# Kernel optimization log

Measured on AMD Instinct MI355X. Metric: run time of the kernel, lower is better.

The kernel has to match this reference:

```python
import jax, jax.numpy as jnp
import numpy as np

N_NODES = 50000
N_EDGES = 800000
IN_CH = 64
OUT_CH = 64
PRIOR_VAR = 1.0


def setup_inputs() -> dict:
    key = jax.random.key(0)
    ks = jax.random.split(key, 10)
    mean = jax.random.normal(ks[0], (N_NODES, IN_CH), dtype=jnp.float32)
    std = jax.random.uniform(ks[1], (N_NODES, IN_CH), dtype=jnp.float32)
    edge_index = jax.random.randint(ks[2], (2, N_EDGES), 0, N_NODES, dtype=jnp.int32)
    edge_weight = jax.random.uniform(ks[3], (N_EDGES,), dtype=jnp.float32)
    # Bayesian GCN parameters (xavier-ish mu, log_sigma init -3.0) for mean- and std-branches
    scale = float(np.sqrt(6.0 / (IN_CH + OUT_CH)))
    mu_mean = jax.random.uniform(ks[4], (IN_CH, OUT_CH), minval=-scale, maxval=scale, dtype=jnp.float32)
    log_sigma_mean = jnp.full((IN_CH, OUT_CH), -3.0, dtype=jnp.float32)
    mu_std = jax.random.uniform(ks[5], (IN_CH, OUT_CH), minval=-scale, maxval=scale, dtype=jnp.float32)
    log_sigma_std = jnp.full((IN_CH, OUT_CH), -3.0, dtype=jnp.float32)
    # reparameterization noise (drawn once so reference is deterministic)
    eps_mean = jax.random.normal(ks[6], (IN_CH, OUT_CH), dtype=jnp.float32)
    eps_std = jax.random.normal(ks[7], (IN_CH, OUT_CH), dtype=jnp.float32)
    return {
        "mean": mean, "std": std, "edge_index": edge_index, "edge_weight": edge_weight,
        "mu_mean": mu_mean, "log_sigma_mean": log_sigma_mean, "eps_mean": eps_mean,
        "mu_std": mu_std, "log_sigma_std": log_sigma_std, "eps_std": eps_std,
    }


def _gcn_propagate(x, weight, edge_index, edge_weight):
    # support = x @ W; then gather src rows, scale by edge_weight, scatter-add to dst
    support = jnp.matmul(x, weight)                      # [N, out]
    src, dst = edge_index[0], edge_index[1]
    msg = edge_weight[:, None] * support[src]            # [E, out]
    return jax.ops.segment_sum(msg, dst, num_segments=N_NODES)


def _kl(mu, log_sigma):
    pv = PRIOR_VAR
    kl = 0.5 * (jnp.exp(2.0 * log_sigma) / pv + mu ** 2 / pv
                - 2.0 * log_sigma - jnp.log(jnp.asarray(pv, mu.dtype)) - 1.0)
    return kl.sum()


def reference(mean, std, edge_index, edge_weight,
              mu_mean, log_sigma_mean, eps_mean,
              mu_std, log_sigma_std, eps_std):
    # mean branch
    w_mean = mu_mean + eps_mean * jnp.exp(log_sigma_mean)
    new_mean = _gcn_propagate(mean, w_mean, edge_index, edge_weight)
    kl_mean = _kl(mu_mean, log_sigma_mean)
    # std branch operates on variance with squared edge weights
    var = std ** 2
    w_std = mu_std + eps_std * jnp.exp(log_sigma_std)
    new_log_var = _gcn_propagate(var, w_std, edge_index, edge_weight ** 2)
    kl_std = _kl(mu_std, log_sigma_std)
    new_std = jnp.sqrt(jnp.exp(new_log_var) + 1e-6)
    total_kl = kl_mean + kl_std
    return (new_mean, new_std, total_kl)
```

## Files before the change

kernel.cpp:

```cpp
#include <hip/hip_runtime.h>

#define N_NODES 50000
#define N_EDGES 800000
#define CH 64
#define OUT_OFF_STD (N_NODES * CH)
#define OUT_OFF_KL  (2 * N_NODES * CH)
#define CAP 64
#define CAP_USE 62

#define NGRP 8
#define NPG 6250
#define FILL_CHUNK 4096
#define FILL_CHUNKS 196
#define FILL_BLOCKS (NGRP * FILL_CHUNKS)
#define GEMM_BLOCKS 782
#define GATHER_BLOCKS 2048
#define GWAVES_PG 1024
#define ZERO_GRID 208

typedef __attribute__((ext_vector_type(8))) short short8;
typedef __attribute__((ext_vector_type(4))) float f32x4;

__device__ __forceinline__ int rl_i(unsigned v, int lane) {
    return __builtin_amdgcn_readlane((int)v, lane);
}
__device__ __forceinline__ unsigned f2bf(float f) {
    unsigned u = __float_as_uint(f);
    return (u + 0x7fffu + ((u >> 16) & 1u)) >> 16;
}
__device__ __forceinline__ int* cnt_ptr(uint2* bins, int node) {
    return (int*)(bins + (size_t)node * CAP + 63);
}

__global__ __launch_bounds__(256) void wkl_kernel(
    const float* __restrict__ mu_m, const float* __restrict__ ls_m,
    const float* __restrict__ eps_m,
    const float* __restrict__ mu_s, const float* __restrict__ ls_s,
    const float* __restrict__ eps_s,
    unsigned short* __restrict__ fragBm, unsigned short* __restrict__ fragBv,
    float* __restrict__ kl_out, uint2* __restrict__ bins)
{
    if (blockIdx.x != 0) {
        if (blockIdx.x < 8) return;
        const int g = blockIdx.x & (NGRP - 1);
        const int loc = ((int)(blockIdx.x >> 3) - 1) * 256 + (int)threadIdx.x;
        if (loc < NPG) *cnt_ptr(bins, g * NPG + loc) = 0;
        return;
    }
    __shared__ unsigned short Wm[CH * CH];
    __shared__ unsigned short Wv[CH * CH];
    float kl = 0.0f;
    for (int i = threadIdx.x; i < CH * CH; i += 256) {
        float mu = mu_m[i], ls = ls_m[i];
        Wm[i] = (unsigned short)f2bf(mu + eps_m[i] * expf(ls));
        kl += 0.5f * (expf(2.0f * ls) + mu * mu - 2.0f * ls - 1.0f);
        mu = mu_s[i]; ls = ls_s[i];
        Wv[i] = (unsigned short)f2bf(mu + eps_s[i] * expf(ls));
        kl += 0.5f * (expf(2.0f * ls) + mu * mu - 2.0f * ls - 1.0f);
    }
    __syncthreads();
    for (int f = threadIdx.x; f < CH * CH; f += 256) {
        int j = f & 7, l = (f >> 3) & 63, ch = f >> 9;
        int k = (ch & 1) * 32 + ((l >> 4) & 3) * 8 + j;
        int n = (ch >> 1) * 16 + (l & 15);
        fragBm[f] = Wm[k * CH + n];
        fragBv[f] = Wv[k * CH + n];
    }
    for (int off = 32; off > 0; off >>= 1)
        kl += __shfl_down(kl, off, 64);
    __shared__ float red[4];
    if ((threadIdx.x & 63) == 0) red[threadIdx.x >> 6] = kl;
    __syncthreads();
    if (threadIdx.x == 0)
        kl_out[0] = red[0] + red[1] + red[2] + red[3];
}

__global__ __launch_bounds__(256) void gemfill_kernel(
    const float* __restrict__ mean, const float* __restrict__ stdv,
    const unsigned short* __restrict__ fragBm,
    const unsigned short* __restrict__ fragBv,
    const int* __restrict__ ei, const float* __restrict__ ew,
    uint2* __restrict__ bins, unsigned* __restrict__ sup)
{
    const int tid = threadIdx.x;

    if (blockIdx.x < FILL_BLOCKS) {
        const int g = blockIdx.x & (NGRP - 1);
        const int chunk = blockIdx.x >> 3;
        const int base = chunk * FILL_CHUNK + tid * 16;
        const int lo = g * NPG;

        int d[16], s[16]; float w[16];
        if (base + 16 <= N_EDGES) {
#pragma unroll
            for (int h = 0; h < 4; ++h) {
                int4 dv = *(const int4*)(ei + N_EDGES + base + h * 4);
                d[h * 4 + 0] = dv.x; d[h * 4 + 1] = dv.y;
                d[h * 4 + 2] = dv.z; d[h * 4 + 3] = dv.w;
            }
#pragma unroll
            for (int h = 0; h < 4; ++h) {
                int4 sv = *(const int4*)(ei + base + h * 4);
                s[h * 4 + 0] = sv.x; s[h * 4 + 1] = sv.y;
                s[h * 4 + 2] = sv.z; s[h * 4 + 3] = sv.w;
            }
#pragma unroll
            for (int h = 0; h < 4; ++h) {
                float4 wv = *(const float4*)(ew + base + h * 4);
                w[h * 4 + 0] = wv.x; w[h * 4 + 1] = wv.y;
                w[h * 4 + 2] = wv.z; w[h * 4 + 3] = wv.w;
            }
        } else {
#pragma unroll
            for (int t = 0; t < 16; ++t) {
                bool v = (base + t) < N_EDGES;
                d[t] = v ? ei[N_EDGES + base + t] : -1;
                s[t] = v ? ei[base + t] : 0;
                w[t] = v ? ew[base + t] : 0.0f;
            }
        }

        int slot[16];
#pragma unroll
        for (int t = 0; t < 16; ++t) {
            bool act = (unsigned)(d[t] - lo) < (unsigned)NPG;
            slot[t] = act ? atomicAdd(cnt_ptr(bins, d[t]), 1) : CAP;
        }
#pragma unroll
        for (int t = 0; t < 16; ++t) {
            if (slot[t] < CAP_USE)
                bins[(size_t)d[t] * CAP + slot[t]] =
                    make_uint2((unsigned)s[t], __float_as_uint(w[t]));
        }
        return;
    }

    const int lane = tid & 63, wave = tid >> 6;
    const int row0 = (blockIdx.x - FILL_BLOCKS) * 64 + wave * 16;
    if (row0 >= N_NODES) return;

    const int m = lane & 15;
    const int q = (lane >> 4) & 3;
    const float* mrow = mean + (size_t)(row0 + m) * CH + q * 8;
    const float* srow = stdv + (size_t)(row0 + m) * CH + q * 8;

    short8 aM[2], aV[2];
#pragma unroll
    for (int h = 0; h < 2; ++h) {
        float4 x0 = *(const float4*)(mrow + h * 32);
        float4 x1 = *(const float4*)(mrow + h * 32 + 4);
        float4 s0 = *(const float4*)(srow + h * 32);
        float4 s1 = *(const float4*)(srow + h * 32 + 4);
        aM[h][0] = (short)f2bf(x0.x); aM[h][1] = (short)f2bf(x0.y);
        aM[h][2] = (short)f2bf(x0.z); aM[h][3] = (short)f2bf(x0.w);
        aM[h][4] = (short)f2bf(x1.x); aM[h][5] = (short)f2bf(x1.y);
        aM[h][6] = (short)f2bf(x1.z); aM[h][7] = (short)f2bf(x1.w);
        aV[h][0] = (short)f2bf(s0.x * s0.x); aV[h][1] = (short)f2bf(s0.y * s0.y);
        aV[h][2] = (short)f2bf(s0.z * s0.z); aV[h][3] = (short)f2bf(s0.w * s0.w);
        aV[h][4] = (short)f2bf(s1.x * s1.x); aV[h][5] = (short)f2bf(s1.y * s1.y);
        aV[h][6] = (short)f2bf(s1.z * s1.z); aV[h][7] = (short)f2bf(s1.w * s1.w);
    }

    f32x4 accM[4], accV[4];
#pragma unroll
    for (int c = 0; c < 4; ++c) {
        accM[c] = (f32x4)0.0f;
        accV[c] = (f32x4)0.0f;
    }
#pragma unroll
    for (int c = 0; c < 4; ++c) {
#pragma unroll
        for (int h = 0; h < 2; ++h) {
            short8 bm = *(const short8*)(fragBm + ((c * 2 + h) * 64 + lane) * 8);
            short8 bv = *(const short8*)(fragBv + ((c * 2 + h) * 64 + lane) * 8);
            accM[c] = __builtin_amdgcn_mfma_f32_16x16x32_bf16(aM[h], bm, accM[c], 0, 0, 0);
            accV[c] = __builtin_amdgcn_mfma_f32_16x16x32_bf16(aV[h], bv, accV[c], 0, 0, 0);
        }
    }

    const int rg = lane >> 4;
#pragma unroll
    for (int c = 0; c < 4; ++c) {
#pragma unroll
        for (int r = 0; r < 4; ++r) {
            int node = row0 + rg * 4 + r;
            sup[(size_t)node * CH + c * 16 + m] =
                f2bf(accM[c][r]) | (f2bf(accV[c][r]) << 16);
        }
    }
}

__global__ __launch_bounds__(256) void gather_kernel(
    const uint2* __restrict__ bins,
    const unsigned* __restrict__ sup, float* __restrict__ out)
{
    const int g = blockIdx.x & (NGRP - 1);
    const int wid = ((int)(blockIdx.x >> 3)) * 4 + (int)(threadIdx.x >> 6);
    const int col = threadIdx.x & 63;
    const int nbase = g * NPG;

    int loc = wid;
    if (loc >= NPG) return;

    uint2 pnext = bins[(size_t)(nbase + loc) * CAP + col];

    for (; loc < NPG; loc += GWAVES_PG) {
        uint2 p = pnext;
        {
            int loc2 = loc + GWAVES_PG;
            if (loc2 < NPG)
                pnext = bins[(size_t)(nbase + loc2) * CAP + col];
        }
        int cnt = rl_i(p.x, 63);
        if (cnt > CAP_USE) cnt = CAP_USE;

        float accM = 0.0f, accV = 0.0f;
        if (cnt > 0) {
            unsigned q[24];
#pragma unroll
            for (int t = 0; t < 24; ++t) {
                int e = (t < cnt) ? t : (cnt - 1);
                q[t] = sup[(size_t)(unsigned)rl_i(p.x, e) * CH + col];
            }
#pragma unroll
            for (int t = 0; t < 24; ++t) {
                int e = (t < cnt) ? t : (cnt - 1);
                float wt = (t < cnt)
                    ? __uint_as_float((unsigned)rl_i(p.y, e)) : 0.0f;
                accM += wt * __uint_as_float(q[t] << 16);
                accV += (wt * wt) * __uint_as_float(q[t] & 0xFFFF0000u);
            }
            for (int i = 24; i < cnt; i += 8) {
                unsigned qq[8]; float ww[8];
#pragma unroll
                for (int t = 0; t < 8; ++t) {
                    int e = (i + t < cnt) ? (i + t) : (cnt - 1);
                    qq[t] = sup[(size_t)(unsigned)rl_i(p.x, e) * CH + col];
                    ww[t] = (i + t < cnt)
                        ? __uint_as_float((unsigned)rl_i(p.y, e)) : 0.0f;
                }
#pragma unroll
                for (int t = 0; t < 8; ++t) {
                    accM += ww[t] * __uint_as_float(qq[t] << 16);
                    accV += (ww[t] * ww[t]) * __uint_as_float(qq[t] & 0xFFFF0000u);
                }
            }
        }
        const int n = nbase + loc;
        __builtin_nontemporal_store(accM, &out[(size_t)n * CH + col]);
        __builtin_nontemporal_store(sqrtf(expf(accV) + 1e-6f),
                                    &out[OUT_OFF_STD + (size_t)n * CH + col]);
    }
}

extern "C" void kernel_launch(void* const* d_in, const int* in_sizes, int n_in,
                              void* d_out, int out_size, void* d_ws, size_t ws_size,
                              hipStream_t stream)
{
    const float* mean  = (const float*)d_in[0];
    const float* stdv  = (const float*)d_in[1];
    const int*   ei    = (const int*)d_in[2];
    const float* ew    = (const float*)d_in[3];
    const float* mu_m  = (const float*)d_in[4];
    const float* ls_m  = (const float*)d_in[5];
    const float* eps_m = (const float*)d_in[6];
    const float* ls_s  = (const float*)d_in[8];
    const float* mu_s  = (const float*)d_in[7];
    const float* eps_s = (const float*)d_in[9];

    float* out = (float*)d_out;
    unsigned*       sup    = (unsigned*)d_ws;
    uint2*          bins   = (uint2*)(sup + (size_t)N_NODES * CH);
    unsigned short* fragBm = (unsigned short*)(bins + (size_t)N_NODES * CAP);
    unsigned short* fragBv = fragBm + CH * CH;

    wkl_kernel<<<ZERO_GRID, 256, 0, stream>>>(
        mu_m, ls_m, eps_m, mu_s, ls_s, eps_s,
        fragBm, fragBv, out + OUT_OFF_KL, bins);
    gemfill_kernel<<<FILL_BLOCKS + GEMM_BLOCKS, 256, 0, stream>>>(
        mean, stdv, fragBm, fragBv, ei, ew, bins, sup);
    gather_kernel<<<GATHER_BLOCKS, 256, 0, stream>>>(bins, sup, out);
}
```

Measured before the change: 174.4 us.

## Fuse three kernels into one persistent cooperative kernel with grid syncs

```diff
diff --git a/kernel.cpp b/kernel.cpp
--- a/kernel.cpp
+++ b/kernel.cpp
@@ -1,4 +1,7 @@
 #include <hip/hip_runtime.h>
+#include <hip/hip_cooperative_groups.h>
+
+namespace cg = cooperative_groups;
 
 #define N_NODES 50000
 #define N_EDGES 800000
@@ -10,13 +13,10 @@
 
 #define NGRP 8
 #define NPG 6250
-#define FILL_CHUNK 4096
-#define FILL_CHUNKS 196
-#define FILL_BLOCKS (NGRP * FILL_CHUNKS)
-#define GEMM_BLOCKS 782
-#define GATHER_BLOCKS 2048
-#define GWAVES_PG 1024
-#define ZERO_GRID 208
+#define FILL_CHUNK 2048
+#define FILL_CHUNKS 391
+#define GEMM_TILES 782
+#define MAX_BLOCKS 1536
 
 typedef __attribute__((ext_vector_type(8))) short short8;
 typedef __attribute__((ext_vector_type(4))) float f32x4;
@@ -32,224 +32,221 @@
     return (int*)(bins + (size_t)node * CAP + 63);
 }
 
-__global__ __launch_bounds__(256) void wkl_kernel(
+__global__ __launch_bounds__(256, 6) void fused_kernel(
+    const float* __restrict__ mean, const float* __restrict__ stdv,
+    const int* __restrict__ ei, const float* __restrict__ ew,
     const float* __restrict__ mu_m, const float* __restrict__ ls_m,
     const float* __restrict__ eps_m,
     const float* __restrict__ mu_s, const float* __restrict__ ls_s,
     const float* __restrict__ eps_s,
     unsigned short* __restrict__ fragBm, unsigned short* __restrict__ fragBv,
-    float* __restrict__ kl_out, uint2* __restrict__ bins)
+    uint2* __restrict__ bins, unsigned* __restrict__ sup,
+    int* __restrict__ qcnt, float* __restrict__ out)
 {
-    if (blockIdx.x != 0) {
-        if (blockIdx.x < 8) return;
-        const int g = blockIdx.x & (NGRP - 1);
-        const int loc = ((int)(blockIdx.x >> 3) - 1) * 256 + (int)threadIdx.x;
-        if (loc < NPG) *cnt_ptr(bins, g * NPG + loc) = 0;
-        return;
+    cg::grid_group grid = cg::this_grid();
+    const int tid = threadIdx.x;
+    const int bid = (int)blockIdx.x;
+    const int nblk = (int)gridDim.x;
+
+    __shared__ float red[4];
+    __shared__ int sh_chunk;
+
+    if (bid == 0) {
+        float kl = 0.0f;
+        for (int i = tid; i < CH * CH; i += 256) {
+            float mu = mu_m[i], ls = ls_m[i];
+            kl += 0.5f * (expf(2.0f * ls) + mu * mu - 2.0f * ls - 1.0f);
+            mu = mu_s[i]; ls = ls_s[i];
+            kl += 0.5f * (expf(2.0f * ls) + mu * mu - 2.0f * ls - 1.0f);
+        }
+        for (int off = 32; off > 0; off >>= 1)
+            kl += __shfl_down(kl, off, 64);
+        if ((tid & 63) == 0) red[tid >> 6] = kl;
+        __syncthreads();
+        if (tid == 0)
+            out[OUT_OFF_KL] = red[0] + red[1] + red[2] + red[3];
+    } else {
+        const int p = (bid - 1) * 256 + tid;
+        const int pstride = (nblk - 1) * 256;
+        for (int f = p; f < CH * CH; f += pstride) {
+            int j = f & 7, l = (f >> 3) & 63, ch = f >> 9;
+            int k = (ch & 1) * 32 + ((l >> 4) & 3) * 8 + j;
+            int n = (ch >> 1) * 16 + (l & 15);
+            int i = k * CH + n;
+            fragBm[f] = (unsigned short)f2bf(mu_m[i] + eps_m[i] * expf(ls_m[i]));
+            fragBv[f] = (unsigned short)f2bf(mu_s[i] + eps_s[i] * expf(ls_s[i]));
+        }
+        for (int i = p; i < N_NODES; i += pstride)
+            *cnt_ptr(bins, i) = 0;
+        if (p < NGRP * 16) qcnt[p] = 0;
     }
-    __shared__ unsigned short Wm[CH * CH];
-    __shared__ unsigned short Wv[CH * CH];
-    float kl = 0.0f;
-    for (int i = threadIdx.x; i < CH * CH; i += 256) {
-        float mu = mu_m[i], ls = ls_m[i];
-        Wm[i] = (unsigned short)f2bf(mu + eps_m[i] * expf(ls));
-        kl += 0.5f * (expf(2.0f * ls) + mu * mu - 2.0f * ls - 1.0f);
-        mu = mu_s[i]; ls = ls_s[i];
-        Wv[i] = (unsigned short)f2bf(mu + eps_s[i] * expf(ls));
-        kl += 0.5f * (expf(2.0f * ls) + mu * mu - 2.0f * ls - 1.0f);
+    grid.sync();
+
+    const int gb = nblk >> 3;
+    const int fb = nblk - gb;
+    if (bid < fb) {
+        const int g = bid & (NGRP - 1);
+        const int lo = g * NPG;
+        for (;;) {
+            __syncthreads();
+            if (tid == 0) sh_chunk = atomicAdd(&qcnt[g * 16], 1);
+            __syncthreads();
+            const int c = sh_chunk;
+            if (c >= FILL_CHUNKS) break;
+            const int base = c * FILL_CHUNK + tid * 8;
+
+            int d[8], s[8]; float w[8];
+            if (base + 8 <= N_EDGES) {
+                int4 d0 = *(const int4*)(ei + N_EDGES + base);
+                int4 d1 = *(const int4*)(ei + N_EDGES + base + 4);
+                d[0] = d0.x; d[1] = d0.y; d[2] = d0.z; d[3] = d0.w;
+                d[4] = d1.x; d[5] = d1.y; d[6] = d1.z; d[7] = d1.w;
+                int4 s0 = *(const int4*)(ei + base);
+                int4 s1 = *(const int4*)(ei + base + 4);
+                s[0] = s0.x; s[1] = s0.y; s[2] = s0.z; s[3] = s0.w;
+                s[4] = s1.x; s[5] = s1.y; s[6] = s1.z; s[7] = s1.w;
+                float4 w0 = *(const float4*)(ew + base);
+                float4 w1 = *(const float4*)(ew + base + 4);
+                w[0] = w0.x; w[1] = w0.y; w[2] = w0.z; w[3] = w0.w;
+                w[4] = w1.x; w[5] = w1.y; w[6] = w1.z; w[7] = w1.w;
+            } else {
+#pragma unroll
+                for (int t = 0; t < 8; ++t) {
+                    bool v = (base + t) < N_EDGES;
+                    d[t] = v ? ei[N_EDGES + base + t] : -1;
+                    s[t] = v ? ei[base + t] : 0;
+                    w[t] = v ? ew[base + t] : 0.0f;
+                }
+            }
+            int slot[8];
+#pragma unroll
+            for (int t = 0; t < 8; ++t) {
+                bool act = (unsigned)(d[t] - lo) < (unsigned)NPG;
+                slot[t] = act ? atomicAdd(cnt_ptr(bins, d[t]), 1) : CAP;
+            }
+#pragma unroll
+            for (int t = 0; t < 8; ++t) {
+                if (slot[t] < CAP_USE)
+                    bins[(size_t)d[t] * CAP + slot[t]] =
+                        make_uint2((unsigned)s[t], __float_as_uint(w[t]));
+            }
+        }
+    } else {
+        const int lane = tid & 63, wave = tid >> 6;
+        const int m = lane & 15;
+        const int q = (lane >> 4) & 3;
+        const int rg = lane >> 4;
+
+        for (int t = bid - fb; t < GEMM_TILES; t += gb) {
+            const int row0 = t * 64 + wave * 16;
+            if (row0 >= N_NODES) continue;
+            const float* mrow = mean + (size_t)(row0 + m) * CH + q * 8;
+            const float* srow = stdv + (size_t)(row0 + m) * CH + q * 8;
+
+            short8 aM[2], aV[2];
+#pragma unroll
+            for (int h = 0; h < 2; ++h) {
+                float4 x0 = *(const float4*)(mrow + h * 32);
+                float4 x1 = *(const float4*)(mrow + h * 32 + 4);
+                float4 s0 = *(const float4*)(srow + h * 32);
+                float4 s1 = *(const float4*)(srow + h * 32 + 4);
+                aM[h][0] = (short)f2bf(x0.x); aM[h][1] = (short)f2bf(x0.y);
+                aM[h][2] = (short)f2bf(x0.z); aM[h][3] = (short)f2bf(x0.w);
+                aM[h][4] = (short)f2bf(x1.x); aM[h][5] = (short)f2bf(x1.y);
+                aM[h][6] = (short)f2bf(x1.z); aM[h][7] = (short)f2bf(x1.w);
+                aV[h][0] = (short)f2bf(s0.x * s0.x); aV[h][1] = (short)f2bf(s0.y * s0.y);
+                aV[h][2] = (short)f2bf(s0.z * s0.z); aV[h][3] = (short)f2bf(s0.w * s0.w);
+                aV[h][4] = (short)f2bf(s1.x * s1.x); aV[h][5] = (short)f2bf(s1.y * s1.y);
+                aV[h][6] = (short)f2bf(s1.z * s1.z); aV[h][7] = (short)f2bf(s1.w * s1.w);
+            }
+
+            f32x4 accM[4], accV[4];
+#pragma unroll
+            for (int c = 0; c < 4; ++c) {
+                accM[c] = (f32x4)0.0f;
+                accV[c] = (f32x4)0.0f;
+            }
+#pragma unroll
+            for (int c = 0; c < 4; ++c) {
+#pragma unroll
+                for (int h = 0; h < 2; ++h) {
+                    short8 bm = *(const short8*)(fragBm + ((c * 2 + h) * 64 + lane) * 8);
+                    short8 bv = *(const short8*)(fragBv + ((c * 2 + h) * 64 + lane) * 8);
+                    accM[c] = __builtin_amdgcn_mfma_f32_16x16x32_bf16(aM[h], bm, accM[c], 0, 0, 0);
+                    accV[c] = __builtin_amdgcn_mfma_f32_16x16x32_bf16(aV[h], bv, accV[c], 0, 0, 0);
+                }
+            }
+#pragma unroll
+            for (int c = 0; c < 4; ++c) {
+#pragma unroll
+                for (int r = 0; r < 4; ++r) {
+                    int node = row0 + rg * 4 + r;
+                    sup[(size_t)node * CH + c * 16 + m] =
+                        f2bf(accM[c][r]) | (f2bf(accV[c][r]) << 16);
+                }
+            }
+        }
     }
-    __syncthreads();
-    for (int f = threadIdx.x; f < CH * CH; f += 256) {
-        int j = f & 7, l = (f >> 3) & 63, ch = f >> 9;
-        int k = (ch & 1) * 32 + ((l >> 4) & 3) * 8 + j;
-        int n = (ch >> 1) * 16 + (l & 15);
-        fragBm[f] = Wm[k * CH + n];
-        fragBv[f] = Wv[k * CH + n];
-    }
-    for (int off = 32; off > 0; off >>= 1)
-        kl += __shfl_down(kl, off, 64);
-    __shared__ float red[4];
-    if ((threadIdx.x & 63) == 0) red[threadIdx.x >> 6] = kl;
-    __syncthreads();
-    if (threadIdx.x == 0)
-        kl_out[0] = red[0] + red[1] + red[2] + red[3];
-}
-
-__global__ __launch_bounds__(256) void gemfill_kernel(
-    const float* __restrict__ mean, const float* __restrict__ stdv,
-    const unsigned short* __restrict__ fragBm,
-    const unsigned short* __restrict__ fragBv,
-    const int* __restrict__ ei, const float* __restrict__ ew,
-    uint2* __restrict__ bins, unsigned* __restrict__ sup)
-{
-    const int tid = threadIdx.x;
-
-    if (blockIdx.x < FILL_BLOCKS) {
-        const int g = blockIdx.x & (NGRP - 1);
-        const int chunk = blockIdx.x >> 3;
-        const int base = chunk * FILL_CHUNK + tid * 16;
-        const int lo = g * NPG;
-
-        int d[16], s[16]; float w[16];
-        if (base + 16 <= N_EDGES) {
-#pragma unroll
-            for (int h = 0; h < 4; ++h) {
-                int4 dv = *(const int4*)(ei + N_EDGES + base + h * 4);
-                d[h * 4 + 0] = dv.x; d[h * 4 + 1] = dv.y;
-                d[h * 4 + 2] = dv.z; d[h * 4 + 3] = dv.w;
-            }
-#pragma unroll
-            for (int h = 0; h < 4; ++h) {
-                int4 sv = *(const int4*)(ei + base + h * 4);
-                s[h * 4 + 0] = sv.x; s[h * 4 + 1] = sv.y;
-                s[h * 4 + 2] = sv.z; s[h * 4 + 3] = sv.w;
-            }
-#pragma unroll
-            for (int h = 0; h < 4; ++h) {
-                float4 wv = *(const float4*)(ew + base + h * 4);
-                w[h * 4 + 0] = wv.x; w[h * 4 + 1] = wv.y;
-                w[h * 4 + 2] = wv.z; w[h * 4 + 3] = wv.w;
-            }
-        } else {
-#pragma unroll
-            for (int t = 0; t < 16; ++t) {
-                bool v = (base + t) < N_EDGES;
-                d[t] = v ? ei[N_EDGES + base + t] : -1;
-                s[t] = v ? ei[base + t] : 0;
-                w[t] = v ? ew[base + t] : 0.0f;
-            }
-        }
-
-        int slot[16];
-#pragma unroll
-        for (int t = 0; t < 16; ++t) {
-            bool act = (unsigned)(d[t] - lo) < (unsigned)NPG;
-            slot[t] = act ? atomicAdd(cnt_ptr(bins, d[t]), 1) : CAP;
-        }
-#pragma unroll
-        for (int t = 0; t < 16; ++t) {
-            if (slot[t] < CAP_USE)
-                bins[(size_t)d[t] * CAP + slot[t]] =
-                    make_uint2((unsigned)s[t], __float_as_uint(w[t]));
-        }
-        return;
-    }
-
-    const int lane = tid & 63, wave = tid >> 6;
-    const int row0 = (blockIdx.x - FILL_BLOCKS) * 64 + wave * 16;
-    if (row0 >= N_NODES) return;
-
-    const int m = lane & 15;
-    const int q = (lane >> 4) & 3;
-    const float* mrow = mean + (size_t)(row0 + m) * CH + q * 8;
-    const float* srow = stdv + (size_t)(row0 + m) * CH + q * 8;
-
-    short8 aM[2], aV[2];
-#pragma unroll
-    for (int h = 0; h < 2; ++h) {
-        float4 x0 = *(const float4*)(mrow + h * 32);
-        float4 x1 = *(const float4*)(mrow + h * 32 + 4);
-        float4 s0 = *(const float4*)(srow + h * 32);
-        float4 s1 = *(const float4*)(srow + h * 32 + 4);
-        aM[h][0] = (short)f2bf(x0.x); aM[h][1] = (short)f2bf(x0.y);
-        aM[h][2] = (short)f2bf(x0.z); aM[h][3] = (short)f2bf(x0.w);
-        aM[h][4] = (short)f2bf(x1.x); aM[h][5] = (short)f2bf(x1.y);
-        aM[h][6] = (short)f2bf(x1.z); aM[h][7] = (short)f2bf(x1.w);
-        aV[h][0] = (short)f2bf(s0.x * s0.x); aV[h][1] = (short)f2bf(s0.y * s0.y);
-        aV[h][2] = (short)f2bf(s0.z * s0.z); aV[h][3] = (short)f2bf(s0.w * s0.w);
-        aV[h][4] = (short)f2bf(s1.x * s1.x); aV[h][5] = (short)f2bf(s1.y * s1.y);
-        aV[h][6] = (short)f2bf(s1.z * s1.z); aV[h][7] = (short)f2bf(s1.w * s1.w);
-    }
-
-    f32x4 accM[4], accV[4];
-#pragma unroll
-    for (int c = 0; c < 4; ++c) {
-        accM[c] = (f32x4)0.0f;
-        accV[c] = (f32x4)0.0f;
-    }
-#pragma unroll
-    for (int c = 0; c < 4; ++c) {
-#pragma unroll
-        for (int h = 0; h < 2; ++h) {
-            short8 bm = *(const short8*)(fragBm + ((c * 2 + h) * 64 + lane) * 8);
-            short8 bv = *(const short8*)(fragBv + ((c * 2 + h) * 64 + lane) * 8);
-            accM[c] = __builtin_amdgcn_mfma_f32_16x16x32_bf16(aM[h], bm, accM[c], 0, 0, 0);
-            accV[c] = __builtin_amdgcn_mfma_f32_16x16x32_bf16(aV[h], bv, accV[c], 0, 0, 0);
-        }
-    }
-
-    const int rg = lane >> 4;
-#pragma unroll
-    for (int c = 0; c < 4; ++c) {
-#pragma unroll
-        for (int r = 0; r < 4; ++r) {
-            int node = row0 + rg * 4 + r;
-            sup[(size_t)node * CH + c * 16 + m] =
-                f2bf(accM[c][r]) | (f2bf(accV[c][r]) << 16);
-        }
-    }
-}
-
-__global__ __launch_bounds__(256) void gather_kernel(
-    const uint2* __restrict__ bins,
-    const unsigned* __restrict__ sup, float* __restrict__ out)
-{
-    const int g = blockIdx.x & (NGRP - 1);
-    const int wid = ((int)(blockIdx.x >> 3)) * 4 + (int)(threadIdx.x >> 6);
-    const int col = threadIdx.x & 63;
-    const int nbase = g * NPG;
-
-    int loc = wid;
-    if (loc >= NPG) return;
-
-    uint2 pnext = bins[(size_t)(nbase + loc) * CAP + col];
-
-    for (; loc < NPG; loc += GWAVES_PG) {
-        uint2 p = pnext;
-        {
-            int loc2 = loc + GWAVES_PG;
-            if (loc2 < NPG)
-                pnext = bins[(size_t)(nbase + loc2) * CAP + col];
-        }
-        int cnt = rl_i(p.x, 63);
-        if (cnt > CAP_USE) cnt = CAP_USE;
-
-        float accM = 0.0f, accV = 0.0f;
-        if (cnt > 0) {
-            unsigned q[24];
-#pragma unroll
-            for (int t = 0; t < 24; ++t) {
-                int e = (t < cnt) ? t : (cnt - 1);
-                q[t] = sup[(size_t)(unsigned)rl_i(p.x, e) * CH + col];
-            }
-#pragma unroll
-            for (int t = 0; t < 24; ++t) {
-                int e = (t < cnt) ? t : (cnt - 1);
-                float wt = (t < cnt)
-                    ? __uint_as_float((unsigned)rl_i(p.y, e)) : 0.0f;
-                accM += wt * __uint_as_float(q[t] << 16);
-                accV += (wt * wt) * __uint_as_float(q[t] & 0xFFFF0000u);
-            }
-            for (int i = 24; i < cnt; i += 8) {
-                unsigned qq[8]; float ww[8];
-#pragma unroll
-                for (int t = 0; t < 8; ++t) {
-                    int e = (i + t < cnt) ? (i + t) : (cnt - 1);
-                    qq[t] = sup[(size_t)(unsigned)rl_i(p.x, e) * CH + col];
-                    ww[t] = (i + t < cnt)
-                        ? __uint_as_float((unsigned)rl_i(p.y, e)) : 0.0f;
-                }
-#pragma unroll
-                for (int t = 0; t < 8; ++t) {
-                    accM += ww[t] * __uint_as_float(qq[t] << 16);
-                    accV += (ww[t] * ww[t]) * __uint_as_float(qq[t] & 0xFFFF0000u);
-                }
-            }
-        }
-        const int n = nbase + loc;
-        __builtin_nontemporal_store(accM, &out[(size_t)n * CH + col]);
-        __builtin_nontemporal_store(sqrtf(expf(accV) + 1e-6f),
-                                    &out[OUT_OFF_STD + (size_t)n * CH + col]);
+    grid.sync();
+
+    {
+        const int g = bid & (NGRP - 1);
+        const int wpg = (nblk >> 3) * 4;
+        const int wid = (bid >> 3) * 4 + (tid >> 6);
+        const int col = tid & 63;
+        const int nbase = g * NPG;
+
+        int loc = wid;
+        if (loc < NPG) {
+            uint2 pnext = bins[(size_t)(nbase + loc) * CAP + col];
+            for (; loc < NPG; loc += wpg) {
+                uint2 p = pnext;
+                {
+                    int loc2 = loc + wpg;
+                    if (loc2 < NPG)
+                        pnext = bins[(size_t)(nbase + loc2) * CAP + col];
+                }
+                int cnt = rl_i(p.x, 63);
+                if (cnt > CAP_USE) cnt = CAP_USE;
+
+                float accM = 0.0f, accV = 0.0f;
+                if (cnt > 0) {
+                    unsigned qv[24];
+#pragma unroll
+                    for (int t = 0; t < 24; ++t) {
+                        int e = (t < cnt) ? t : (cnt - 1);
+                        qv[t] = sup[(size_t)(unsigned)rl_i(p.x, e) * CH + col];
+                    }
+#pragma unroll
+                    for (int t = 0; t < 24; ++t) {
+                        int e = (t < cnt) ? t : (cnt - 1);
+                        float wt = (t < cnt)
+                            ? __uint_as_float((unsigned)rl_i(p.y, e)) : 0.0f;
+                        accM += wt * __uint_as_float(qv[t] << 16);
+                        accV += (wt * wt) * __uint_as_float(qv[t] & 0xFFFF0000u);
+                    }
+                    for (int i = 24; i < cnt; i += 8) {
+                        unsigned qq[8]; float ww[8];
+#pragma unroll
+                        for (int t = 0; t < 8; ++t) {
+                            int e = (i + t < cnt) ? (i + t) : (cnt - 1);
+                            qq[t] = sup[(size_t)(unsigned)rl_i(p.x, e) * CH + col];
+                            ww[t] = (i + t < cnt)
+                                ? __uint_as_float((unsigned)rl_i(p.y, e)) : 0.0f;
+                        }
+#pragma unroll
+                        for (int t = 0; t < 8; ++t) {
+                            accM += ww[t] * __uint_as_float(qq[t] << 16);
+                            accV += (ww[t] * ww[t]) * __uint_as_float(qq[t] & 0xFFFF0000u);
+                        }
+                    }
+                }
+                const int n = nbase + loc;
+                __builtin_nontemporal_store(accM, &out[(size_t)n * CH + col]);
+                __builtin_nontemporal_store(sqrtf(expf(accV) + 1e-6f),
+                                            &out[OUT_OFF_STD + (size_t)n * CH + col]);
+            }
+        }
     }
 }
 
@@ -273,11 +270,32 @@
     uint2*          bins   = (uint2*)(sup + (size_t)N_NODES * CH);
     unsigned short* fragBm = (unsigned short*)(bins + (size_t)N_NODES * CAP);
     unsigned short* fragBv = fragBm + CH * CH;
-
-    wkl_kernel<<<ZERO_GRID, 256, 0, stream>>>(
-        mu_m, ls_m, eps_m, mu_s, ls_s, eps_s,
-        fragBm, fragBv, out + OUT_OFF_KL, bins);
-    gemfill_kernel<<<FILL_BLOCKS + GEMM_BLOCKS, 256, 0, stream>>>(
-        mean, stdv, fragBm, fragBv, ei, ew, bins, sup);
-    gather_kernel<<<GATHER_BLOCKS, 256, 0, stream>>>(bins, sup, out);
-}
+    int*            qcnt   = (int*)(fragBv + CH * CH);
+
+    static int nblk_cached = 0;
+    if (nblk_cached == 0) {
+        int maxb = 0;
+        hipOccupancyMaxActiveBlocksPerMultiprocessor(
+            &maxb, (const void*)fused_kernel, 256, 0);
+        if (maxb < 1) maxb = 1;
+        int cu = 256;
+        hipDeviceProp_t prop;
+        if (hipGetDeviceProperties(&prop, 0) == hipSuccess && prop.multiProcessorCount > 0)
+            cu = prop.multiProcessorCount;
+        int nb = maxb * cu;
+        if (nb > MAX_BLOCKS) nb = MAX_BLOCKS;
+        nb &= ~31;
+        if (nb < 32) nb = 32;
+        nblk_cached = nb;
+    }
+
+    void* args[] = {
+        (void*)&mean, (void*)&stdv, (void*)&ei, (void*)&ew,
+        (void*)&mu_m, (void*)&ls_m, (void*)&eps_m,
+        (void*)&mu_s, (void*)&ls_s, (void*)&eps_s,
+        (void*)&fragBm, (void*)&fragBv, (void*)&bins, (void*)&sup,
+        (void*)&qcnt, (void*)&out
+    };
+    hipLaunchCooperativeKernel((const void*)fused_kernel,
+                               dim3(nblk_cached), dim3(256), args, 0, stream);
+}
```

After: 393.3 us. 2.25x slower.

## Replace group-partitioned edge binning with flat per-edge fill blocks

Applied to the files above, without the earlier changes.

```diff
diff --git a/kernel.cpp b/kernel.cpp
--- a/kernel.cpp
+++ b/kernel.cpp
@@ -10,9 +10,8 @@
 
 #define NGRP 8
 #define NPG 6250
-#define FILL_CHUNK 4096
-#define FILL_CHUNKS 196
-#define FILL_BLOCKS (NGRP * FILL_CHUNKS)
+#define EPT 4
+#define FILL_BLOCKS 782
 #define GEMM_BLOCKS 782
 #define GATHER_BLOCKS 2048
 #define GWAVES_PG 1024
@@ -85,34 +84,19 @@
     const int tid = threadIdx.x;
 
     if (blockIdx.x < FILL_BLOCKS) {
-        const int g = blockIdx.x & (NGRP - 1);
-        const int chunk = blockIdx.x >> 3;
-        const int base = chunk * FILL_CHUNK + tid * 16;
-        const int lo = g * NPG;
-
-        int d[16], s[16]; float w[16];
-        if (base + 16 <= N_EDGES) {
-#pragma unroll
-            for (int h = 0; h < 4; ++h) {
-                int4 dv = *(const int4*)(ei + N_EDGES + base + h * 4);
-                d[h * 4 + 0] = dv.x; d[h * 4 + 1] = dv.y;
-                d[h * 4 + 2] = dv.z; d[h * 4 + 3] = dv.w;
-            }
-#pragma unroll
-            for (int h = 0; h < 4; ++h) {
-                int4 sv = *(const int4*)(ei + base + h * 4);
-                s[h * 4 + 0] = sv.x; s[h * 4 + 1] = sv.y;
-                s[h * 4 + 2] = sv.z; s[h * 4 + 3] = sv.w;
-            }
-#pragma unroll
-            for (int h = 0; h < 4; ++h) {
-                float4 wv = *(const float4*)(ew + base + h * 4);
-                w[h * 4 + 0] = wv.x; w[h * 4 + 1] = wv.y;
-                w[h * 4 + 2] = wv.z; w[h * 4 + 3] = wv.w;
-            }
+        const int base = (int)blockIdx.x * (256 * EPT) + tid * EPT;
+
+        int d[EPT], s[EPT]; float w[EPT];
+        if (base + EPT <= N_EDGES) {
+            int4 dv = *(const int4*)(ei + N_EDGES + base);
+            d[0] = dv.x; d[1] = dv.y; d[2] = dv.z; d[3] = dv.w;
+            int4 sv = *(const int4*)(ei + base);
+            s[0] = sv.x; s[1] = sv.y; s[2] = sv.z; s[3] = sv.w;
+            float4 wv = *(const float4*)(ew + base);
+            w[0] = wv.x; w[1] = wv.y; w[2] = wv.z; w[3] = wv.w;
         } else {
 #pragma unroll
-            for (int t = 0; t < 16; ++t) {
+            for (int t = 0; t < EPT; ++t) {
                 bool v = (base + t) < N_EDGES;
                 d[t] = v ? ei[N_EDGES + base + t] : -1;
                 s[t] = v ? ei[base + t] : 0;
@@ -120,14 +104,14 @@
             }
         }
 
-        int slot[16];
-#pragma unroll
-        for (int t = 0; t < 16; ++t) {
-            bool act = (unsigned)(d[t] - lo) < (unsigned)NPG;
+        int slot[EPT];
+#pragma unroll
+        for (int t = 0; t < EPT; ++t) {
+            bool act = (unsigned)d[t] < (unsigned)N_NODES;
             slot[t] = act ? atomicAdd(cnt_ptr(bins, d[t]), 1) : CAP;
         }
 #pragma unroll
-        for (int t = 0; t < 16; ++t) {
+        for (int t = 0; t < EPT; ++t) {
             if (slot[t] < CAP_USE)
                 bins[(size_t)d[t] * CAP + slot[t]] =
                     make_uint2((unsigned)s[t], __float_as_uint(w[t]));
```

Measured after the change: 187.9 us. +7.7%, slower.
